# Kernel optimization log

Hardware: AMD Instinct MI355X
Metric: run time of the kernel (lower is better)

Reference implementation:

```python
import jax, jax.numpy as jnp
import numpy as np


def _edt(mask):
    """Exact Euclidean distance transform of a binary [H,W] mask.

    Matches scipy.ndimage.distance_transform_edt: for nonzero pixels,
    distance to the nearest zero pixel (0 at zero pixels).
    Two-pass exact algorithm: 1D distance along rows (axis 0) per column,
    then D[i,j] = min_k d1[i,k]^2 + (j-k)^2 (Felzenszwalb-Huttenlocher identity).
    """
    H, W = mask.shape
    BIG = jnp.float32(H + W)  # larger than any real pixel distance
    zero = mask == 0
    idx = jnp.arange(H, dtype=jnp.float32)[:, None]  # [H,1]
    # nearest zero above (inclusive)
    up = jax.lax.cummax(jnp.where(zero, idx, -BIG), axis=0)
    d_up = idx - up
    # nearest zero below (inclusive): cummin from the bottom
    dn = -jnp.flip(jax.lax.cummax(jnp.flip(jnp.where(zero, -idx, -2 * BIG), axis=0), axis=0), axis=0)
    d_dn = dn - idx
    d1 = jnp.minimum(jnp.minimum(d_up, d_dn), BIG)  # [H,W] 1D column distance
    d1sq = d1 * d1
    j = jnp.arange(W, dtype=jnp.float32)
    off = (j[:, None] - j[None, :]) ** 2  # [W,W], off[j,k]
    # D[i,j] = min_k d1sq[i,k] + (j-k)^2
    Dsq = jnp.min(d1sq[:, None, :] + off[None, :, :], axis=-1)  # [H,W]
    return jnp.sqrt(Dsq)


def _phi_level_set(mask):
    """Normalized signed distance map for one [H,W] binary mask."""
    dist_inside = _edt(mask)
    dist_outside = _edt(1.0 - mask)
    phi = dist_outside - dist_inside
    denom = jnp.max(jnp.abs(phi)) + 1e-8
    return jnp.where(jnp.any(mask > 0), phi / denom, jnp.zeros_like(phi))


def _combined_loss(predictions, targets):
    probs = jax.nn.sigmoid(predictions)
    # Dice
    p = probs.reshape(-1)
    t = targets.reshape(-1)
    smooth = 1e-6
    inter = jnp.sum(p * t)
    dice = 1.0 - (2.0 * inter + smooth) / (jnp.sum(p) + jnp.sum(t) + smooth)
    # Boundary: phi is computed from detached targets (constant)
    masks = jax.lax.stop_gradient(targets)[:, 0]  # [B,H,W]
    phi = jax.vmap(_phi_level_set)(masks)[:, None]  # [B,1,H,W]
    boundary = jnp.mean(phi * probs)
    # BCE with logits (numerically stable)
    x = predictions
    bce = jnp.mean(jnp.clip(x, 0.0, None) - x * targets + jnp.log1p(jnp.exp(-jnp.abs(x))))
    # rebalance schedule at epoch 0: alpha = initial_alpha = 0.005
    alpha = 0.005
    beta = max(0.0, 0.6 - alpha)
    return (1.0 - beta) * dice + beta * boundary + 0.4 * bce


def setup_inputs() -> dict:
    key = jax.random.key(0)
    k1, k2 = jax.random.split(key)
    B, C, H, W = 16, 1, 256, 256
    predictions = jax.random.normal(k1, (B, C, H, W), dtype=jnp.float32)
    targets = (jax.random.uniform(k2, (B, C, H, W)) < 0.3).astype(jnp.float32)
    return {"predictions": predictions, "targets": targets}


def reference(predictions, targets):
    return _combined_loss(predictions, targets)
```

## Files before the change

kernel.cpp:

```cpp
#include <hip/hip_runtime.h>
#include <math.h>

#define BB 16
#define HH 256
#define WW 256
#define NPIX (BB*HH*WW)
#define CH 16
#define RPC 16
#define ROWS 4
#define NRB (BB*HH/ROWS)
#define GSTRIDE 304


__global__ __launch_bounds__(256) void zbuild_kernel(const float* __restrict__ targ,
                                                     unsigned short* __restrict__ zb) {
    int b = blockIdx.x >> 4;
    int ch = blockIdx.x & 15;
    int j = threadIdx.x;
    const float* m = targ + (b * HH + ch * RPC) * WW + j;
    unsigned z = 0;
    #pragma unroll
    for (int r = 0; r < RPC; ++r)
        if (m[r * WW] == 0.0f) z |= (1u << r);
    zb[blockIdx.x * WW + j] = (unsigned short)z;
}

__global__ __launch_bounds__(256) void rowmin_fused_kernel(const unsigned short* __restrict__ zb,
                                                           const float* __restrict__ pred,
                                                           float* __restrict__ partials) {
    int g = blockIdx.x;
    int b = g >> 6;
    int r0 = (g & 63) << 2;
    int C = r0 >> 4;
    int rb0 = r0 & 15;
    int j = threadIdx.x;

    unsigned zc[CH];
    int anym = 0;
    unsigned zoc = 0;
    #pragma unroll
    for (int c = 0; c < CH; ++c) {
        zc[c] = (unsigned)zb[((b * CH + c) << 8) + j];
        anym |= (((~zc[c]) & 0xFFFFu) != 0u);
        if (c == C) zoc = zc[c];
    }

    float x[ROWS];
    #pragma unroll
    for (int r = 0; r < ROWS; ++r)
        x[r] = pred[(((b << 8) + (r0 + r)) << 8) + j];

    __shared__ float gg[ROWS][2][GSTRIDE];
    {
        int buf = threadIdx.x >> 5;
        int pi = threadIdx.x & 31;
        gg[buf >> 1][buf & 1][(pi < 16) ? pi : (256 + pi)] = 1e30f;
    }

    #pragma unroll
    for (int f = 0; f < 2; ++f) {
        int la = -1, fb = 100000;
        #pragma unroll
        for (int c = 0; c < CH; ++c) {
            unsigned z = f ? ((~zc[c]) & 0xFFFFu) : zc[c];
            if (c < C && z) la = (c << 4) + (31 - __clz(z));
        }
        #pragma unroll
        for (int c = CH - 1; c >= 0; --c) {
            unsigned z = f ? ((~zc[c]) & 0xFFFFu) : zc[c];
            if (c > C && z) fb = (c << 4) + (__ffs(z) - 1);
        }
        unsigned zo = f ? ((~zoc) & 0xFFFFu) : zoc;
        #pragma unroll
        for (int r = 0; r < ROWS; ++r) {
            int rb = rb0 + r;
            int i = r0 + r;
            unsigned below = zo & ((2u << rb) - 1u);
            int lz = below ? ((C << 4) + (31 - __clz(below))) : la;
            unsigned above = zo & (~((1u << rb) - 1u) & 0xFFFFu);
            int fz = above ? ((C << 4) + (__ffs(above) - 1)) : fb;
            int da = (lz < 0) ? 100000 : (i - lz);
            int db = fz - i;
            int d = min(min(da, db), 512);
            float fd = (float)d;
            gg[r][f][16 + j] = fd * fd;
        }
    }
    __syncthreads();

    float sp = 0.f, st = 0.f, spt = 0.f, sbce = 0.f, sphip = 0.f, amax = 0.f;
    #pragma unroll
    for (int r = 0; r < ROWS; ++r) {
        int rb = rb0 + r;
        bool msk = (((zoc >> rb) & 1u) == 0u);
        const float* bsel = &gg[r][msk ? 0 : 1][0];
        float best = 1e30f;
        #pragma unroll
        for (int c = 0; c <= 32; ++c) {
            float Cc = (float)((16 - c) * (16 - c));
            best = fminf(best, bsel[j + c] + Cc);
        }
        if (__any(best > 289.0f)) {
            const float* bs = bsel + 16;
            for (int k = 0; k < WW; ++k) {
                float df = (float)(j - k);
                best = fminf(best, bs[k] + df * df);
            }
        }
        float dd = sqrtf(best);
        float phi = msk ? -dd : dd;
        float xr = x[r];
        float p = 1.0f / (1.0f + expf(-xr));
        sp += p;
        st += msk ? 1.0f : 0.0f;
        spt += msk ? p : 0.0f;
        sbce += fmaxf(xr, 0.0f) - (msk ? xr : 0.0f) + log1pf(expf(-fabsf(xr)));
        sphip += phi * p;
        amax = fmaxf(amax, fabsf(phi));
    }

    float anymf = (float)anym;
    #pragma unroll
    for (int off = 32; off > 0; off >>= 1) {
        sp    += __shfl_down(sp,    off, 64);
        st    += __shfl_down(st,    off, 64);
        spt   += __shfl_down(spt,   off, 64);
        sbce  += __shfl_down(sbce,  off, 64);
        sphip += __shfl_down(sphip, off, 64);
        amax   = fmaxf(amax,  __shfl_down(amax,  off, 64));
        anymf  = fmaxf(anymf, __shfl_down(anymf, off, 64));
    }
    __shared__ float red[4][8];
    int lane = j & 63, wv = j >> 6;
    if (lane == 0) {
        red[wv][0] = sp; red[wv][1] = st; red[wv][2] = spt; red[wv][3] = sbce;
        red[wv][4] = sphip; red[wv][5] = amax; red[wv][6] = anymf;
    }
    __syncthreads();
    if (j == 0) {
        float* o = partials + g * 8;
        #pragma unroll
        for (int q = 0; q < 5; ++q)
            o[q] = red[0][q] + red[1][q] + red[2][q] + red[3][q];
        o[5] = fmaxf(fmaxf(red[0][5], red[1][5]), fmaxf(red[2][5], red[3][5]));
        o[6] = fmaxf(fmaxf(red[0][6], red[1][6]), fmaxf(red[2][6], red[3][6]));
    }
}

__global__ __launch_bounds__(256) void final_kernel(const float* __restrict__ partials,
                                                    float* __restrict__ out) {
    int t = threadIdx.x;
    float s0 = 0.f, s1 = 0.f, s2 = 0.f, s3 = 0.f, s4 = 0.f, m5 = 0.f, a6 = 0.f;
    #pragma unroll
    for (int e = 0; e < 4; ++e) {
        const float* rec = partials + ((t * 4 + e) << 3);
        s0 += rec[0]; s1 += rec[1]; s2 += rec[2]; s3 += rec[3];
        s4 += rec[4];
        m5 = fmaxf(m5, rec[5]);
        a6 = fmaxf(a6, rec[6]);
    }
    __shared__ float arr[256][8];
    arr[t][4] = s4; arr[t][5] = m5; arr[t][6] = a6;
    __syncthreads();
    __shared__ float bnd[16];
    if (t < 16) {
        float Sb = 0.f, Mb = 0.f, Ab = 0.f;
        for (int e = 0; e < 16; ++e) {
            Sb += arr[t * 16 + e][4];
            Mb = fmaxf(Mb, arr[t * 16 + e][5]);
            Ab = fmaxf(Ab, arr[t * 16 + e][6]);
        }
        bnd[t] = (Ab != 0.0f) ? (Sb / (Mb + 1e-8f)) : 0.0f;
    }
    #pragma unroll
    for (int off = 32; off > 0; off >>= 1) {
        s0 += __shfl_down(s0, off, 64);
        s1 += __shfl_down(s1, off, 64);
        s2 += __shfl_down(s2, off, 64);
        s3 += __shfl_down(s3, off, 64);
    }
    __shared__ float wred[4][4];
    int lane = t & 63, wv = t >> 6;
    if (lane == 0) { wred[wv][0] = s0; wred[wv][1] = s1; wred[wv][2] = s2; wred[wv][3] = s3; }
    __syncthreads();
    if (t == 0) {
        float sp   = wred[0][0] + wred[1][0] + wred[2][0] + wred[3][0];
        float st   = wred[0][1] + wred[1][1] + wred[2][1] + wred[3][1];
        float spt  = wred[0][2] + wred[1][2] + wred[2][2] + wred[3][2];
        float sbce = wred[0][3] + wred[1][3] + wred[2][3] + wred[3][3];
        float sbnd = 0.f;
        #pragma unroll
        for (int bb2 = 0; bb2 < BB; ++bb2) sbnd += bnd[bb2];
        float dice = 1.0f - (2.0f * spt + 1e-6f) / (sp + st + 1e-6f);
        float invN = 1.0f / (float)NPIX;
        float boundary = sbnd * invN;
        float bce = sbce * invN;
        float alpha = 0.005f;
        float beta = 0.6f - alpha;
        out[0] = (1.0f - beta) * dice + beta * boundary + 0.4f * bce;
    }
}

extern "C" void kernel_launch(void* const* d_in, const int* in_sizes, int n_in,
                              void* d_out, int out_size, void* d_ws, size_t ws_size,
                              hipStream_t stream) {
    (void)in_sizes; (void)n_in; (void)out_size; (void)ws_size;
    const float* pred = (const float*)d_in[0];
    const float* targ = (const float*)d_in[1];
    unsigned short* zb = (unsigned short*)d_ws;
    float* partials = (float*)((char*)d_ws + BB * CH * WW * sizeof(unsigned short));

    zbuild_kernel<<<BB * CH, 256, 0, stream>>>(targ, zb);
    rowmin_fused_kernel<<<NRB, 256, 0, stream>>>(zb, pred, partials);
    final_kernel<<<1, 256, 0, stream>>>(partials, (float*)d_out);
}
```

Before: 72.86 us.

## Vectorize zero-bit build, double rows per block, shrink EDT window, fast sigmoid

The zero-bitmask build now reads float4 and writes ushort4 using 64-thread blocks. The fused kernel handles 8 rows per block instead of 4, which halves the number of blocks. It computes the nearest-zero bounds for both polarities in one pass over the column bitmasks. The local squared-distance window shrinks from ±16 to ±4, so the full 256-wide fallback scan fires more often. Sigmoid and BCE now use __expf/__logf with a shared exp term, trading accuracy for fewer transcendental calls.

```diff
diff --git a/kernel.cpp b/kernel.cpp
--- a/kernel.cpp
+++ b/kernel.cpp
@@ -7,43 +7,62 @@
 #define NPIX (BB*HH*WW)
 #define CH 16
 #define RPC 16
-#define ROWS 4
+#define ROWS 8
 #define NRB (BB*HH/ROWS)
-#define GSTRIDE 304
-
-
-__global__ __launch_bounds__(256) void zbuild_kernel(const float* __restrict__ targ,
-                                                     unsigned short* __restrict__ zb) {
-    int b = blockIdx.x >> 4;
-    int ch = blockIdx.x & 15;
-    int j = threadIdx.x;
-    const float* m = targ + (b * HH + ch * RPC) * WW + j;
-    unsigned z = 0;
-    #pragma unroll
-    for (int r = 0; r < RPC; ++r)
-        if (m[r * WW] == 0.0f) z |= (1u << r);
-    zb[blockIdx.x * WW + j] = (unsigned short)z;
+#define PADW 4
+#define GSTRIDE (WW + 2*PADW)
+
+
+__global__ __launch_bounds__(64) void zbuild_kernel(const float4* __restrict__ targ4,
+                                                    ushort4* __restrict__ zb4) {
+    int blk = blockIdx.x;
+    int t = threadIdx.x;
+    const float4* m = targ4 + (size_t)blk * RPC * (WW / 4) + t;
+    unsigned z0 = 0, z1 = 0, z2 = 0, z3 = 0;
+    #pragma unroll
+    for (int r = 0; r < RPC; ++r) {
+        float4 v = m[r * (WW / 4)];
+        if (v.x == 0.0f) z0 |= 1u << r;
+        if (v.y == 0.0f) z1 |= 1u << r;
+        if (v.z == 0.0f) z2 |= 1u << r;
+        if (v.w == 0.0f) z3 |= 1u << r;
+    }
+    ushort4 o;
+    o.x = (unsigned short)z0; o.y = (unsigned short)z1;
+    o.z = (unsigned short)z2; o.w = (unsigned short)z3;
+    zb4[blk * (WW / 4) + t] = o;
 }
 
 __global__ __launch_bounds__(256) void rowmin_fused_kernel(const unsigned short* __restrict__ zb,
                                                            const float* __restrict__ pred,
                                                            float* __restrict__ partials) {
     int g = blockIdx.x;
-    int b = g >> 6;
-    int r0 = (g & 63) << 2;
+    int b = g >> 5;
+    int r0 = (g & 31) << 3;
     int C = r0 >> 4;
     int rb0 = r0 & 15;
     int j = threadIdx.x;
 
-    unsigned zc[CH];
+    int la0 = -1, la1 = -1;
+    int fb0 = 100000, fb1 = 100000;
+    unsigned zoc = 0;
     int anym = 0;
-    unsigned zoc = 0;
     #pragma unroll
     for (int c = 0; c < CH; ++c) {
-        zc[c] = (unsigned)zb[((b * CH + c) << 8) + j];
-        anym |= (((~zc[c]) & 0xFFFFu) != 0u);
-        if (c == C) zoc = zc[c];
-    }
+        unsigned z = (unsigned)zb[((b * CH + c) << 8) + j];
+        unsigned zi = (~z) & 0xFFFFu;
+        anym |= (zi != 0u);
+        if (c < C) {
+            if (z)  la0 = (c << 4) + (31 - __clz(z));
+            if (zi) la1 = (c << 4) + (31 - __clz(zi));
+        } else if (c > C) {
+            if (z  && fb0 == 100000) fb0 = (c << 4) + (__ffs(z) - 1);
+            if (zi && fb1 == 100000) fb1 = (c << 4) + (__ffs(zi) - 1);
+        } else {
+            zoc = z;
+        }
+    }
+    unsigned zoc1 = (~zoc) & 0xFFFFu;
 
     float x[ROWS];
     #pragma unroll
@@ -51,40 +70,31 @@
         x[r] = pred[(((b << 8) + (r0 + r)) << 8) + j];
 
     __shared__ float gg[ROWS][2][GSTRIDE];
-    {
-        int buf = threadIdx.x >> 5;
-        int pi = threadIdx.x & 31;
-        gg[buf >> 1][buf & 1][(pi < 16) ? pi : (256 + pi)] = 1e30f;
-    }
-
-    #pragma unroll
-    for (int f = 0; f < 2; ++f) {
-        int la = -1, fb = 100000;
-        #pragma unroll
-        for (int c = 0; c < CH; ++c) {
-            unsigned z = f ? ((~zc[c]) & 0xFFFFu) : zc[c];
-            if (c < C && z) la = (c << 4) + (31 - __clz(z));
-        }
-        #pragma unroll
-        for (int c = CH - 1; c >= 0; --c) {
-            unsigned z = f ? ((~zc[c]) & 0xFFFFu) : zc[c];
-            if (c > C && z) fb = (c << 4) + (__ffs(z) - 1);
-        }
-        unsigned zo = f ? ((~zoc) & 0xFFFFu) : zoc;
-        #pragma unroll
-        for (int r = 0; r < ROWS; ++r) {
-            int rb = rb0 + r;
-            int i = r0 + r;
-            unsigned below = zo & ((2u << rb) - 1u);
-            int lz = below ? ((C << 4) + (31 - __clz(below))) : la;
-            unsigned above = zo & (~((1u << rb) - 1u) & 0xFFFFu);
-            int fz = above ? ((C << 4) + (__ffs(above) - 1)) : fb;
-            int da = (lz < 0) ? 100000 : (i - lz);
-            int db = fz - i;
-            int d = min(min(da, db), 512);
-            float fd = (float)d;
-            gg[r][f][16 + j] = fd * fd;
-        }
+    if (j < 2 * ROWS * 2 * PADW) {
+        int r = j >> 4, f = (j >> 3) & 1, p = j & 7;
+        gg[r][f][(p < PADW) ? p : (WW + p)] = 1e30f;
+    }
+
+    #pragma unroll
+    for (int r = 0; r < ROWS; ++r) {
+        int rb = rb0 + r;
+        int i = r0 + r;
+        unsigned below = zoc & ((2u << rb) - 1u);
+        int lz = below ? ((C << 4) + (31 - __clz(below))) : la0;
+        unsigned above = zoc & (0xFFFFu & ~((1u << rb) - 1u));
+        int fz = above ? ((C << 4) + (__ffs(above) - 1)) : fb0;
+        int da = (lz < 0) ? 100000 : (i - lz);
+        int d0 = min(min(da, fz - i), 512);
+        float f0 = (float)d0;
+        gg[r][0][PADW + j] = f0 * f0;
+        unsigned below1 = zoc1 & ((2u << rb) - 1u);
+        int lz1 = below1 ? ((C << 4) + (31 - __clz(below1))) : la1;
+        unsigned above1 = zoc1 & (0xFFFFu & ~((1u << rb) - 1u));
+        int fz1 = above1 ? ((C << 4) + (__ffs(above1) - 1)) : fb1;
+        int da1 = (lz1 < 0) ? 100000 : (i - lz1);
+        int d1v = min(min(da1, fz1 - i), 512);
+        float f1 = (float)d1v;
+        gg[r][1][PADW + j] = f1 * f1;
     }
     __syncthreads();
 
@@ -96,12 +106,12 @@
         const float* bsel = &gg[r][msk ? 0 : 1][0];
         float best = 1e30f;
         #pragma unroll
-        for (int c = 0; c <= 32; ++c) {
-            float Cc = (float)((16 - c) * (16 - c));
+        for (int c = 0; c <= 2 * PADW; ++c) {
+            float Cc = (float)((PADW - c) * (PADW - c));
             best = fminf(best, bsel[j + c] + Cc);
         }
-        if (__any(best > 289.0f)) {
-            const float* bs = bsel + 16;
+        if (__any(best > 25.0f)) {
+            const float* bs = bsel + PADW;
             for (int k = 0; k < WW; ++k) {
                 float df = (float)(j - k);
                 best = fminf(best, bs[k] + df * df);
@@ -110,11 +120,14 @@
         float dd = sqrtf(best);
         float phi = msk ? -dd : dd;
         float xr = x[r];
-        float p = 1.0f / (1.0f + expf(-xr));
+        float ax = fabsf(xr);
+        float q = __expf(-ax);
+        float pa = 1.0f / (1.0f + q);
+        float p = (xr >= 0.0f) ? pa : q * pa;
         sp += p;
         st += msk ? 1.0f : 0.0f;
         spt += msk ? p : 0.0f;
-        sbce += fmaxf(xr, 0.0f) - (msk ? xr : 0.0f) + log1pf(expf(-fabsf(xr)));
+        sbce += fmaxf(xr, 0.0f) - (msk ? xr : 0.0f) - __logf(pa);
         sphip += phi * p;
         amax = fmaxf(amax, fabsf(phi));
     }
@@ -140,8 +153,8 @@
     if (j == 0) {
         float* o = partials + g * 8;
         #pragma unroll
-        for (int q = 0; q < 5; ++q)
-            o[q] = red[0][q] + red[1][q] + red[2][q] + red[3][q];
+        for (int q2 = 0; q2 < 5; ++q2)
+            o[q2] = red[0][q2] + red[1][q2] + red[2][q2] + red[3][q2];
         o[5] = fmaxf(fmaxf(red[0][5], red[1][5]), fmaxf(red[2][5], red[3][5]));
         o[6] = fmaxf(fmaxf(red[0][6], red[1][6]), fmaxf(red[2][6], red[3][6]));
     }
@@ -152,23 +165,23 @@
     int t = threadIdx.x;
     float s0 = 0.f, s1 = 0.f, s2 = 0.f, s3 = 0.f, s4 = 0.f, m5 = 0.f, a6 = 0.f;
     #pragma unroll
-    for (int e = 0; e < 4; ++e) {
-        const float* rec = partials + ((t * 4 + e) << 3);
+    for (int e = 0; e < 2; ++e) {
+        const float* rec = partials + ((t * 2 + e) << 3);
         s0 += rec[0]; s1 += rec[1]; s2 += rec[2]; s3 += rec[3];
         s4 += rec[4];
         m5 = fmaxf(m5, rec[5]);
         a6 = fmaxf(a6, rec[6]);
     }
-    __shared__ float arr[256][8];
-    arr[t][4] = s4; arr[t][5] = m5; arr[t][6] = a6;
+    __shared__ float arr[256][3];
+    arr[t][0] = s4; arr[t][1] = m5; arr[t][2] = a6;
     __syncthreads();
     __shared__ float bnd[16];
     if (t < 16) {
         float Sb = 0.f, Mb = 0.f, Ab = 0.f;
         for (int e = 0; e < 16; ++e) {
-            Sb += arr[t * 16 + e][4];
-            Mb = fmaxf(Mb, arr[t * 16 + e][5]);
-            Ab = fmaxf(Ab, arr[t * 16 + e][6]);
+            Sb += arr[t * 16 + e][0];
+            Mb = fmaxf(Mb, arr[t * 16 + e][1]);
+            Ab = fmaxf(Ab, arr[t * 16 + e][2]);
         }
         bnd[t] = (Ab != 0.0f) ? (Sb / (Mb + 1e-8f)) : 0.0f;
     }
@@ -210,7 +223,7 @@
     unsigned short* zb = (unsigned short*)d_ws;
     float* partials = (float*)((char*)d_ws + BB * CH * WW * sizeof(unsigned short));
 
-    zbuild_kernel<<<BB * CH, 256, 0, stream>>>(targ, zb);
+    zbuild_kernel<<<BB * CH, 64, 0, stream>>>((const float4*)targ, (ushort4*)zb);
     rowmin_fused_kernel<<<NRB, 256, 0, stream>>>(zb, pred, partials);
     final_kernel<<<1, 256, 0, stream>>>(partials, (float*)d_out);
 }
```

New measurement: 71.93 us. No clear change (-1.3%).
